# Kernel tuning notes

Hardware: AMD Instinct MI355X
Metric: run time of the kernel (lower is better)

## Reference

```python
import jax, jax.numpy as jnp
import numpy as np


def setup_inputs() -> dict:
    key = jax.random.key(0)
    k1, k2, k3, k4 = jax.random.split(key, 4)
    B, C, H, W = 8, 3, 1024, 2048
    M, h, w = 32, H // 8, W // 8
    img = jax.random.uniform(k1, (B, C, H, W), dtype=jnp.float32)
    planar_masks = jax.random.normal(k2, (B, M, h, w), dtype=jnp.float32)
    disp = jax.random.uniform(k3, (B, h, w), dtype=jnp.float32) * 0.9 + 0.1
    K = jnp.array([[721.5, 0.0, w / 2.0], [0.0, 721.5, h / 2.0], [0.0, 0.0, 1.0]], dtype=jnp.float32)
    intrs = jnp.tile(K[None], (B, 1, 1))
    baseline = jax.random.uniform(k4, (B,), dtype=jnp.float32) * 0.4 + 0.3
    return {"img": img, "planar_masks": planar_masks, "disp": disp, "intrs": intrs, "baseline": baseline}


def reference(img, planar_masks, disp, intrs, baseline):
    B, C, H, W = img.shape
    _, M, h, w = planar_masks.shape
    dt = img.dtype

    # disp -> depth (b,h,w)
    focal = (intrs[:, 0, 0] + intrs[:, 1, 1]) * 0.5
    depth = baseline[:, None, None] * focal[:, None, None] / (disp * 2048.0)

    # depth -> normals via 3x3 Sobel-style central differences, zero padding
    dp = jnp.pad(depth, ((0, 0), (1, 1), (1, 1)))
    gx = 0.5 * (dp[:, 1:-1, 2:] - dp[:, 1:-1, :-2])
    gy = 0.5 * (dp[:, 2:, 1:-1] - dp[:, :-2, 1:-1])
    dir_map = jnp.stack([-gx, -gy, jnp.ones_like(gx)], axis=1)  # (B,3,h,w)
    normal = dir_map / jnp.sqrt(jnp.sum(dir_map ** 2, axis=1, keepdims=True))

    # softmax-weighted per-plane depth/normal (faithful torch .view memory layout)
    wts = jax.nn.softmax(planar_masks.reshape(B, M, h * w), axis=-1)  # (B,M,hw)
    flat_depth = depth.reshape(B, h * w, 1)
    flat_normal = normal.reshape(B, h * w, 3)  # channel-major flatten, as in source
    planar_depth = wts @ flat_depth   # (B,M,1)
    planar_normal = wts @ flat_normal  # (B,M,3)

    # per-plane homographies H = K (R - t n^T / d) K^-1
    R = jnp.broadcast_to(jnp.eye(3, dtype=dt), (B, 3, 3))
    t = jnp.zeros((B, 3, 1), dt).at[:, 2, 0].set(-baseline)
    K_inv = jnp.linalg.inv(intrs)
    tn = t[:, None] @ planar_normal[:, :, None, :]            # (B,M,3,3)
    H_cal = R[:, None] - tn / planar_depth[..., None]
    Hm = intrs[:, None] @ H_cal @ K_inv[:, None]              # (B,M,3,3)

    img_p = img.reshape(B, C, h, 8, w, 8).mean(axis=(3, 5))  # (B,C,h,w)

    # affine_grid (align_corners=True) with the top 2 rows of H
    ys = jnp.linspace(-1.0, 1.0, h, dtype=dt)
    xs = jnp.linspace(-1.0, 1.0, w, dtype=dt)
    gyy, gxx = jnp.meshgrid(ys, xs, indexing="ij")
    base = jnp.stack([gxx, gyy, jnp.ones_like(gxx)], axis=-1)  # (h,w,3)
    grid = jnp.einsum("bmij,hwj->bmhwi", Hm[:, :, :2, :], base)  # (B,M,h,w,2)

    # bilinear grid_sample, zeros padding, align_corners=True
    ix = (grid[..., 0] + 1.0) * (w - 1) * 0.5
    iy = (grid[..., 1] + 1.0) * (h - 1) * 0.5
    x0 = jnp.floor(ix)
    y0 = jnp.floor(iy)
    wx1 = ix - x0
    wy1 = iy - y0
    imgT = img_p.transpose(0, 2, 3, 1)  # (B,h,w,C)
    bidx = jnp.arange(B)[:, None, None, None]

    def corner(xf, yf):
        valid = (xf >= 0) & (xf <= w - 1) & (yf >= 0) & (yf <= h - 1)
        xi = jnp.clip(xf, 0, w - 1).astype(jnp.int32)
        yi = jnp.clip(yf, 0, h - 1).astype(jnp.int32)
        return imgT[bidx, yi, xi] * valid[..., None].astype(dt)  # (B,M,h,w,C)

    warp = (corner(x0, y0) * ((1 - wx1) * (1 - wy1))[..., None]
            + corner(x0 + 1, y0) * (wx1 * (1 - wy1))[..., None]
            + corner(x0, y0 + 1) * ((1 - wx1) * wy1)[..., None]
            + corner(x0 + 1, y0 + 1) * (wx1 * wy1)[..., None])  # (B,M,h,w,C)

    blend = jax.nn.softmax(planar_masks, axis=1)  # (B,M,h,w)
    return jnp.einsum("bmhwc,bmhw->bchw", warp, blend)
```

## Files before the change

### kernel.cpp

```cpp
#include <hip/hip_runtime.h>
#include <math.h>

#define Bq   8
#define Cc   3
#define Hh   128
#define Ww   256
#define Mm   32
#define HW   (Hh*Ww)
#define HIMG 1024
#define WIMG 2048

__global__ void k_depth_normal(const float* __restrict__ disp,
                               const float* __restrict__ intrs,
                               const float* __restrict__ baseline,
                               float* __restrict__ depth,
                               float* __restrict__ normal) {
    int idx = blockIdx.x * blockDim.x + threadIdx.x;
    int b = idx >> 15;
    int p = idx & (HW - 1);
    int y = p >> 8;
    int x = p & (Ww - 1);
    float focal = 0.5f * (intrs[b * 9 + 0] + intrs[b * 9 + 4]);
    float k = baseline[b] * focal * (1.0f / 2048.0f);
    const float* db = disp + (size_t)b * HW;
    float Dc  = k / db[p];
    float Dxm = (x > 0)      ? k / db[p - 1]  : 0.0f;
    float Dxp = (x < Ww - 1) ? k / db[p + 1]  : 0.0f;
    float Dym = (y > 0)      ? k / db[p - Ww] : 0.0f;
    float Dyp = (y < Hh - 1) ? k / db[p + Ww] : 0.0f;
    float gx = 0.5f * (Dxp - Dxm);
    float gy = 0.5f * (Dyp - Dym);
    float invn = 1.0f / sqrtf(gx * gx + gy * gy + 1.0f);
    depth[idx] = Dc;
    float* nb = normal + (size_t)b * 3 * HW;
    nb[p]          = -gx * invn;
    nb[HW + p]     = -gy * invn;
    nb[2 * HW + p] =  invn;
}

__device__ __forceinline__ float blk_reduce(float v, float* lds, bool is_max) {
    #pragma unroll
    for (int off = 32; off; off >>= 1) {
        float o = __shfl_down(v, off, 64);
        v = is_max ? fmaxf(v, o) : (v + o);
    }
    int lane = threadIdx.x & 63, wid = threadIdx.x >> 6;
    if (lane == 0) lds[wid] = v;
    __syncthreads();
    if (threadIdx.x == 0) {
        float r = lds[0];
        for (int i = 1; i < 4; i++) r = is_max ? fmaxf(r, lds[i]) : (r + lds[i]);
        lds[0] = r;
    }
    __syncthreads();
    float r = lds[0];
    __syncthreads();
    return r;
}

__global__ void k_planes(const float* __restrict__ masks,
                         const float* __restrict__ depth,
                         const float* __restrict__ normal,
                         const float* __restrict__ intrs,
                         const float* __restrict__ baseline,
                         float* __restrict__ hm) {
    __shared__ float lds[8];
    int bm = blockIdx.x;
    int b = bm >> 5;
    const float* mp = masks + (size_t)bm * HW;
    const float* dp = depth + (size_t)b * HW;
    const float* np = normal + (size_t)b * 3 * HW;
    int tid = threadIdx.x;

    float mx = -INFINITY;
    for (int p = tid; p < HW; p += 256) mx = fmaxf(mx, mp[p]);
    mx = blk_reduce(mx, lds, true);

    float se = 0.f, sd = 0.f, s0 = 0.f, s1 = 0.f, s2 = 0.f;
    for (int p = tid; p < HW; p += 256) {
        float e = expf(mp[p] - mx);
        se += e;
        sd += e * dp[p];
        s0 += e * np[3 * p];
        s1 += e * np[3 * p + 1];
        s2 += e * np[3 * p + 2];
    }
    se = blk_reduce(se, lds, false);
    sd = blk_reduce(sd, lds, false);
    s0 = blk_reduce(s0, lds, false);
    s1 = blk_reduce(s1, lds, false);
    s2 = blk_reduce(s2, lds, false);

    if (tid == 0) {
        float inv_se = 1.0f / se;
        float pd = sd * inv_se;
        float n0 = s0 * inv_se, n1 = s1 * inv_se, n2 = s2 * inv_se;
        const float* Km = intrs + b * 9;
        float a = Km[0], bb = Km[1], c = Km[2];
        float d = Km[3], e  = Km[4], f = Km[5];
        float g = Km[6], h2 = Km[7], i = Km[8];
        float det = a * (e * i - f * h2) - bb * (d * i - f * g) + c * (d * h2 - e * g);
        float invd = 1.0f / det;
        float ki[9] = {(e * i - f * h2) * invd, (c * h2 - bb * i) * invd, (bb * f - c * e) * invd,
                       (f * g - d * i) * invd, (a * i - c * g) * invd,  (c * d - a * f) * invd,
                       (d * h2 - e * g) * invd, (bb * g - a * h2) * invd, (a * e - bb * d) * invd};
        float s = baseline[b] / pd;
        float A[9] = {1.f, 0.f, 0.f, 0.f, 1.f, 0.f, s * n0, s * n1, 1.0f + s * n2};
        float T[9];
        #pragma unroll
        for (int r = 0; r < 3; r++)
            #pragma unroll
            for (int cc = 0; cc < 3; cc++)
                T[r * 3 + cc] = Km[r * 3 + 0] * A[cc] + Km[r * 3 + 1] * A[3 + cc] + Km[r * 3 + 2] * A[6 + cc];
        #pragma unroll
        for (int r = 0; r < 2; r++)
            #pragma unroll
            for (int cc = 0; cc < 3; cc++)
                hm[bm * 6 + r * 3 + cc] = T[r * 3 + 0] * ki[cc] + T[r * 3 + 1] * ki[3 + cc] + T[r * 3 + 2] * ki[6 + cc];
    }
}

__global__ void k_pool(const float* __restrict__ img, float* __restrict__ img_p) {
    int blk = blockIdx.x;
    int x = threadIdx.x;
    const float* base = img + (size_t)blk * 8 * WIMG;
    float s = 0.f;
    #pragma unroll
    for (int r = 0; r < 8; r++) {
        const float4* rp = (const float4*)(base + (size_t)r * WIMG) + x * 2;
        float4 u = rp[0], v = rp[1];
        s += u.x + u.y + u.z + u.w + v.x + v.y + v.z + v.w;
    }
    img_p[(size_t)blk * Ww + x] = s * (1.0f / 64.0f);
}

__global__ void k_blend(const float* __restrict__ masks,
                        const float* __restrict__ hm,
                        const float* __restrict__ img_p,
                        float* __restrict__ out) {
    int bi = blockIdx.x;
    int b = bi >> 7;
    int y = bi & (Hh - 1);
    int x = threadIdx.x;
    __shared__ float hs[Mm * 6];
    if (x < Mm * 6) hs[x] = hm[b * Mm * 6 + x];
    __syncthreads();

    const float* mp = masks + (size_t)b * Mm * HW + (size_t)y * Ww + x;
    float mv[Mm];
    float mmax = -INFINITY;
    #pragma unroll
    for (int m = 0; m < Mm; m++) {
        mv[m] = mp[(size_t)m * HW];
        mmax = fmaxf(mmax, mv[m]);
    }

    float xn = (2.0f * x - (float)(Ww - 1)) * (1.0f / (float)(Ww - 1));
    float yn = (2.0f * y - (float)(Hh - 1)) * (1.0f / (float)(Hh - 1));
    const float* ip = img_p + (size_t)b * 3 * HW;

    float se = 0.f, a0 = 0.f, a1 = 0.f, a2 = 0.f;
    for (int m = 0; m < Mm; m++) {
        float e = expf(mv[m] - mmax);
        se += e;
        float gx = hs[m * 6 + 0] * xn + hs[m * 6 + 1] * yn + hs[m * 6 + 2];
        float gy = hs[m * 6 + 3] * xn + hs[m * 6 + 4] * yn + hs[m * 6 + 5];
        float ix = (gx + 1.0f) * ((float)(Ww - 1) * 0.5f);
        float iy = (gy + 1.0f) * ((float)(Hh - 1) * 0.5f);
        float x0f = floorf(ix), y0f = floorf(iy);
        float wx1 = ix - x0f, wy1 = iy - y0f;
        float wx0 = 1.0f - wx1, wy0 = 1.0f - wy1;
        float w00 = wx0 * wy0 * e, w10 = wx1 * wy0 * e;
        float w01 = wx0 * wy1 * e, w11 = wx1 * wy1 * e;
        #define CORNER(xf, yf, wt) do {                                              \
            float _xf = (xf), _yf = (yf);                                            \
            if (_xf >= 0.0f && _xf <= (float)(Ww - 1) &&                             \
                _yf >= 0.0f && _yf <= (float)(Hh - 1)) {                             \
                int o = (int)_yf * Ww + (int)_xf;                                    \
                a0 += (wt) * ip[o];                                                  \
                a1 += (wt) * ip[HW + o];                                             \
                a2 += (wt) * ip[2 * HW + o];                                         \
            }                                                                        \
        } while (0)
        CORNER(x0f,        y0f,        w00);
        CORNER(x0f + 1.0f, y0f,        w10);
        CORNER(x0f,        y0f + 1.0f, w01);
        CORNER(x0f + 1.0f, y0f + 1.0f, w11);
        #undef CORNER
    }
    float inv = 1.0f / se;
    int o = y * Ww + x;
    float* ob = out + (size_t)b * 3 * HW;
    ob[o]          = a0 * inv;
    ob[HW + o]     = a1 * inv;
    ob[2 * HW + o] = a2 * inv;
}

extern "C" void kernel_launch(void* const* d_in, const int* in_sizes, int n_in,
                              void* d_out, int out_size, void* d_ws, size_t ws_size,
                              hipStream_t stream) {
    const float* img      = (const float*)d_in[0];
    const float* masks    = (const float*)d_in[1];
    const float* disp     = (const float*)d_in[2];
    const float* intrs    = (const float*)d_in[3];
    const float* baseline = (const float*)d_in[4];
    float* out = (float*)d_out;

    float* depth  = (float*)d_ws;
    float* normal = depth + (size_t)Bq * HW;
    float* hm     = normal + (size_t)Bq * 3 * HW;
    float* img_p  = hm + (size_t)Bq * Mm * 6;

    hipLaunchKernelGGL(k_depth_normal, dim3(Bq * HW / 256), dim3(256), 0, stream,
                       disp, intrs, baseline, depth, normal);
    hipLaunchKernelGGL(k_planes, dim3(Bq * Mm), dim3(256), 0, stream,
                       masks, depth, normal, intrs, baseline, hm);
    hipLaunchKernelGGL(k_pool, dim3(Bq * Cc * Hh), dim3(256), 0, stream,
                       img, img_p);
    hipLaunchKernelGGL(k_blend, dim3(Bq * Hh), dim3(256), 0, stream,
                       masks, hm, img_p, out);
}
```

Before: 388.9 us.

## Interleave pooled image as float4, widen plane reduction blocks, branchless bilinear gather

The pooled image is now stored as interleaved RGB float4 per pixel, so each bilinear corner in the blend kernel needs one 16-byte load instead of three scattered loads. The corner check becomes branchless, with clamped indices and a zero weight for invalid corners, and the blend kernel switches to fast exp and fma. The plane-softmax kernel moves from 256 to 1024 threads per block and merges its five sum reductions behind a single barrier. This adds a fourth padding channel to the workspace and trades exact expf for __expf.

```diff
diff --git a/kernel.cpp b/kernel.cpp
--- a/kernel.cpp
+++ b/kernel.cpp
@@ -38,63 +38,69 @@
     nb[2 * HW + p] =  invn;
 }
 
-__device__ __forceinline__ float blk_reduce(float v, float* lds, bool is_max) {
-    #pragma unroll
-    for (int off = 32; off; off >>= 1) {
-        float o = __shfl_down(v, off, 64);
-        v = is_max ? fmaxf(v, o) : (v + o);
-    }
-    int lane = threadIdx.x & 63, wid = threadIdx.x >> 6;
-    if (lane == 0) lds[wid] = v;
-    __syncthreads();
-    if (threadIdx.x == 0) {
-        float r = lds[0];
-        for (int i = 1; i < 4; i++) r = is_max ? fmaxf(r, lds[i]) : (r + lds[i]);
-        lds[0] = r;
-    }
-    __syncthreads();
-    float r = lds[0];
-    __syncthreads();
-    return r;
-}
-
-__global__ void k_planes(const float* __restrict__ masks,
-                         const float* __restrict__ depth,
-                         const float* __restrict__ normal,
-                         const float* __restrict__ intrs,
-                         const float* __restrict__ baseline,
-                         float* __restrict__ hm) {
-    __shared__ float lds[8];
+__global__ __launch_bounds__(1024) void k_planes(
+        const float* __restrict__ masks,
+        const float* __restrict__ depth,
+        const float* __restrict__ normal,
+        const float* __restrict__ intrs,
+        const float* __restrict__ baseline,
+        float* __restrict__ hm) {
+    __shared__ float lds[5][16];
     int bm = blockIdx.x;
     int b = bm >> 5;
     const float* mp = masks + (size_t)bm * HW;
     const float* dp = depth + (size_t)b * HW;
     const float* np = normal + (size_t)b * 3 * HW;
     int tid = threadIdx.x;
+    int lane = tid & 63, wid = tid >> 6;
 
     float mx = -INFINITY;
-    for (int p = tid; p < HW; p += 256) mx = fmaxf(mx, mp[p]);
-    mx = blk_reduce(mx, lds, true);
+    for (int p = tid; p < HW; p += 1024) mx = fmaxf(mx, mp[p]);
+    #pragma unroll
+    for (int off = 32; off; off >>= 1) mx = fmaxf(mx, __shfl_down(mx, off, 64));
+    if (lane == 0) lds[0][wid] = mx;
+    __syncthreads();
+    if (tid == 0) {
+        float r = lds[0][0];
+        #pragma unroll
+        for (int i = 1; i < 16; i++) r = fmaxf(r, lds[0][i]);
+        lds[0][0] = r;
+    }
+    __syncthreads();
+    mx = lds[0][0];
+    __syncthreads();
 
     float se = 0.f, sd = 0.f, s0 = 0.f, s1 = 0.f, s2 = 0.f;
-    for (int p = tid; p < HW; p += 256) {
-        float e = expf(mp[p] - mx);
+    for (int p = tid; p < HW; p += 1024) {
+        float e = __expf(mp[p] - mx);
         se += e;
-        sd += e * dp[p];
-        s0 += e * np[3 * p];
-        s1 += e * np[3 * p + 1];
-        s2 += e * np[3 * p + 2];
-    }
-    se = blk_reduce(se, lds, false);
-    sd = blk_reduce(sd, lds, false);
-    s0 = blk_reduce(s0, lds, false);
-    s1 = blk_reduce(s1, lds, false);
-    s2 = blk_reduce(s2, lds, false);
+        sd = fmaf(e, dp[p], sd);
+        s0 = fmaf(e, np[3 * p],     s0);
+        s1 = fmaf(e, np[3 * p + 1], s1);
+        s2 = fmaf(e, np[3 * p + 2], s2);
+    }
+    float vals[5] = {se, sd, s0, s1, s2};
+    #pragma unroll
+    for (int j = 0; j < 5; j++) {
+        float v = vals[j];
+        #pragma unroll
+        for (int off = 32; off; off >>= 1) v += __shfl_down(v, off, 64);
+        if (lane == 0) lds[j][wid] = v;
+    }
+    __syncthreads();
 
     if (tid == 0) {
-        float inv_se = 1.0f / se;
-        float pd = sd * inv_se;
-        float n0 = s0 * inv_se, n1 = s1 * inv_se, n2 = s2 * inv_se;
+        float t[5];
+        #pragma unroll
+        for (int j = 0; j < 5; j++) {
+            float r = 0.f;
+            #pragma unroll
+            for (int i = 0; i < 16; i++) r += lds[j][i];
+            t[j] = r;
+        }
+        float inv_se = 1.0f / t[0];
+        float pd = t[1] * inv_se;
+        float n0 = t[2] * inv_se, n1 = t[3] * inv_se, n2 = t[4] * inv_se;
         const float* Km = intrs + b * 9;
         float a = Km[0], bb = Km[1], c = Km[2];
         float d = Km[3], e  = Km[4], f = Km[5];
@@ -120,23 +126,29 @@
     }
 }
 
-__global__ void k_pool(const float* __restrict__ img, float* __restrict__ img_p) {
-    int blk = blockIdx.x;
+__global__ void k_pool(const float* __restrict__ img, float4* __restrict__ img_p) {
+    int bi = blockIdx.x;
+    int b = bi >> 7, y = bi & (Hh - 1);
     int x = threadIdx.x;
-    const float* base = img + (size_t)blk * 8 * WIMG;
-    float s = 0.f;
-    #pragma unroll
-    for (int r = 0; r < 8; r++) {
-        const float4* rp = (const float4*)(base + (size_t)r * WIMG) + x * 2;
-        float4 u = rp[0], v = rp[1];
-        s += u.x + u.y + u.z + u.w + v.x + v.y + v.z + v.w;
-    }
-    img_p[(size_t)blk * Ww + x] = s * (1.0f / 64.0f);
+    float s[3];
+    #pragma unroll
+    for (int c = 0; c < 3; c++) {
+        const float* base = img + ((size_t)(b * 3 + c) * HIMG + (size_t)y * 8) * WIMG + x * 8;
+        float acc = 0.f;
+        #pragma unroll
+        for (int r = 0; r < 8; r++) {
+            float4 u = *(const float4*)(base + (size_t)r * WIMG);
+            float4 v = *(const float4*)(base + (size_t)r * WIMG + 4);
+            acc += u.x + u.y + u.z + u.w + v.x + v.y + v.z + v.w;
+        }
+        s[c] = acc * (1.0f / 64.0f);
+    }
+    img_p[(size_t)bi * Ww + x] = make_float4(s[0], s[1], s[2], 0.f);
 }
 
 __global__ void k_blend(const float* __restrict__ masks,
                         const float* __restrict__ hm,
-                        const float* __restrict__ img_p,
+                        const float4* __restrict__ img_p,
                         float* __restrict__ out) {
     int bi = blockIdx.x;
     int b = bi >> 7;
@@ -157,14 +169,15 @@
 
     float xn = (2.0f * x - (float)(Ww - 1)) * (1.0f / (float)(Ww - 1));
     float yn = (2.0f * y - (float)(Hh - 1)) * (1.0f / (float)(Hh - 1));
-    const float* ip = img_p + (size_t)b * 3 * HW;
+    const float4* ip = img_p + (size_t)b * HW;
 
     float se = 0.f, a0 = 0.f, a1 = 0.f, a2 = 0.f;
+    #pragma unroll 4
     for (int m = 0; m < Mm; m++) {
-        float e = expf(mv[m] - mmax);
+        float e = __expf(mv[m] - mmax);
         se += e;
-        float gx = hs[m * 6 + 0] * xn + hs[m * 6 + 1] * yn + hs[m * 6 + 2];
-        float gy = hs[m * 6 + 3] * xn + hs[m * 6 + 4] * yn + hs[m * 6 + 5];
+        float gx = fmaf(hs[m * 6 + 0], xn, fmaf(hs[m * 6 + 1], yn, hs[m * 6 + 2]));
+        float gy = fmaf(hs[m * 6 + 3], xn, fmaf(hs[m * 6 + 4], yn, hs[m * 6 + 5]));
         float ix = (gx + 1.0f) * ((float)(Ww - 1) * 0.5f);
         float iy = (gy + 1.0f) * ((float)(Hh - 1) * 0.5f);
         float x0f = floorf(ix), y0f = floorf(iy);
@@ -174,13 +187,16 @@
         float w01 = wx0 * wy1 * e, w11 = wx1 * wy1 * e;
         #define CORNER(xf, yf, wt) do {                                              \
             float _xf = (xf), _yf = (yf);                                            \
-            if (_xf >= 0.0f && _xf <= (float)(Ww - 1) &&                             \
-                _yf >= 0.0f && _yf <= (float)(Hh - 1)) {                             \
-                int o = (int)_yf * Ww + (int)_xf;                                    \
-                a0 += (wt) * ip[o];                                                  \
-                a1 += (wt) * ip[HW + o];                                             \
-                a2 += (wt) * ip[2 * HW + o];                                         \
-            }                                                                        \
+            bool _v = (_xf >= 0.0f) && (_xf <= (float)(Ww - 1)) &&                   \
+                      (_yf >= 0.0f) && (_yf <= (float)(Hh - 1));                     \
+            float _xc = fminf(fmaxf(_xf, 0.0f), (float)(Ww - 1));                    \
+            float _yc = fminf(fmaxf(_yf, 0.0f), (float)(Hh - 1));                    \
+            int _o = (int)_yc * Ww + (int)_xc;                                       \
+            float4 _t = ip[_o];                                                      \
+            float _w = _v ? (wt) : 0.0f;                                             \
+            a0 = fmaf(_w, _t.x, a0);                                                 \
+            a1 = fmaf(_w, _t.y, a1);                                                 \
+            a2 = fmaf(_w, _t.z, a2);                                                 \
         } while (0)
         CORNER(x0f,        y0f,        w00);
         CORNER(x0f + 1.0f, y0f,        w10);
@@ -209,13 +225,13 @@
     float* depth  = (float*)d_ws;
     float* normal = depth + (size_t)Bq * HW;
     float* hm     = normal + (size_t)Bq * 3 * HW;
-    float* img_p  = hm + (size_t)Bq * Mm * 6;
+    float4* img_p = (float4*)(hm + (size_t)Bq * Mm * 6);
 
     hipLaunchKernelGGL(k_depth_normal, dim3(Bq * HW / 256), dim3(256), 0, stream,
                        disp, intrs, baseline, depth, normal);
-    hipLaunchKernelGGL(k_planes, dim3(Bq * Mm), dim3(256), 0, stream,
+    hipLaunchKernelGGL(k_planes, dim3(Bq * Mm), dim3(1024), 0, stream,
                        masks, depth, normal, intrs, baseline, hm);
-    hipLaunchKernelGGL(k_pool, dim3(Bq * Cc * Hh), dim3(256), 0, stream,
+    hipLaunchKernelGGL(k_pool, dim3(Bq * Hh), dim3(256), 0, stream,
                        img, img_p);
     hipLaunchKernelGGL(k_blend, dim3(Bq * Hh), dim3(256), 0, stream,
                        masks, hm, img_p, out);
```

After: 346.4 us. -10.9%, faster.
